# Performance work log

Measured on AMD Instinct MI355X. Metric: run time of the kernel, lower is better.

Reference implementation:

```python
import jax, jax.numpy as jnp
import numpy as np

S = 4            # n_streams
SINK_ITERS = 20
EPS = 1e-8
LN_EPS = 1e-5


def sinkhorn_knopp(logits):
    # Project onto doubly stochastic manifold (fixed 20 iterations, tiny SxS matrix)
    P = jnp.exp(logits - jnp.max(logits))
    for _ in range(SINK_ITERS):
        P = P / (jnp.sum(P, axis=-1, keepdims=True) + EPS)
        P = P / (jnp.sum(P, axis=-2, keepdims=True) + EPS)
    return P


def layer_norm(x, gamma, beta):
    mu = jnp.mean(x, axis=-1, keepdims=True)
    var = jnp.mean(jnp.square(x - mu), axis=-1, keepdims=True)
    return (x - mu) * jax.lax.rsqrt(var + LN_EPS) * gamma + beta


def mhc_residual(x_s, layer_s, H_res_logits, H_post_logits, scales):
    # x_{l+1} streams = H_res @ x + H_post.T @ layer_output (per-stream mixing)
    H_res = sinkhorn_knopp(H_res_logits)
    H_post = jax.nn.softmax(H_post_logits, axis=-1)
    residual = jnp.einsum('bnsd,st->bntd', x_s, H_res)
    mixed = jnp.einsum('bnsd,ts->bntd', layer_s, H_post)
    return residual + scales[None, None, :, None] * mixed


def setup_inputs() -> dict:
    key = jax.random.key(0)
    ks = jax.random.split(key, 10)
    B, N, D = 4, 4096, 2048
    scale_w = 1.0 / np.sqrt(D)
    return {
        'x': jax.random.normal(ks[0], (B, N, D), jnp.float32),
        'ln_gamma': jnp.ones((D,), jnp.float32),
        'ln_beta': jnp.zeros((D,), jnp.float32),
        'W_attn': jax.random.normal(ks[1], (D, D), jnp.float32) * scale_w,
        'b_attn': jnp.zeros((D,), jnp.float32),
        'W_hyb': jax.random.normal(ks[2], (D, D), jnp.float32) * scale_w,
        'b_hyb': jnp.zeros((D,), jnp.float32),
        'H_pre_attn_logits': 0.02 * jax.random.normal(ks[3], (S, S), jnp.float32),
        'H_pre_hyb_logits': 0.02 * jax.random.normal(ks[4], (S, S), jnp.float32),
        'H_res_attn_logits': jnp.eye(S, dtype=jnp.float32) + 0.1 * jax.random.normal(ks[5], (S, S), jnp.float32),
        'H_post_attn_logits': 0.02 * jax.random.normal(ks[6], (S, S), jnp.float32),
        'scales_attn': jnp.ones((S,), jnp.float32),
        'H_res_hyb_logits': jnp.eye(S, dtype=jnp.float32) + 0.1 * jax.random.normal(ks[7], (S, S), jnp.float32),
        'H_post_hyb_logits': 0.02 * jax.random.normal(ks[8], (S, S), jnp.float32),
        'scales_hyb': jnp.ones((S,), jnp.float32),
        'cross_mix': jnp.float32(0.5),
    }


def reference(x, ln_gamma, ln_beta, W_attn, b_attn, W_hyb, b_hyb,
              H_pre_attn_logits, H_pre_hyb_logits,
              H_res_attn_logits, H_post_attn_logits, scales_attn,
              H_res_hyb_logits, H_post_hyb_logits, scales_hyb, cross_mix):
    B, N, D = x.shape
    sd = D // S
    x_s = x.reshape(B, N, S, sd)

    # --- attention path: H_pre on LayerNorm-ed input ---
    normed_s = layer_norm(x, ln_gamma, ln_beta).reshape(B, N, S, sd)
    H_pre_attn = jax.nn.softmax(H_pre_attn_logits, axis=-1)
    attn_in = jnp.einsum('bnsd,st->bntd', normed_s, H_pre_attn).reshape(B, N, D)
    attn_out = attn_in @ W_attn + b_attn                  # attn_module stand-in
    x_attn = mhc_residual(x_s, attn_out.reshape(B, N, S, sd),
                          H_res_attn_logits, H_post_attn_logits, scales_attn)

    # --- hybrid path: H_pre on raw x ---
    H_pre_hyb = jax.nn.softmax(H_pre_hyb_logits, axis=-1)
    hyb_in = jnp.einsum('bnsd,st->bntd', x_s, H_pre_hyb).reshape(B, N, D)
    ssm_out = hyb_in @ W_hyb + b_hyb                      # hybrid_module stand-in
    x_hyb = mhc_residual(x_s, ssm_out.reshape(B, N, S, sd),
                         H_res_hyb_logits, H_post_hyb_logits, scales_hyb)

    alpha = jax.nn.sigmoid(cross_mix)
    out = alpha * x_attn + (1.0 - alpha) * x_hyb
    return out.reshape(B, N, D)
```

## Files before the change

kernel.cpp:

```cpp
#include <hip/hip_runtime.h>
#include <stdint.h>

typedef float  f32x4  __attribute__((ext_vector_type(4)));
typedef short  bf16x8 __attribute__((ext_vector_type(8)));
typedef unsigned short u16;
typedef unsigned short u16x8 __attribute__((ext_vector_type(8)));

#define GLD16(gsrc, ldst) \
  __builtin_amdgcn_global_load_lds((const __attribute__((address_space(1))) uint32_t*)(gsrc), \
                                   (__attribute__((address_space(3))) uint32_t*)(ldst), 16, 0, 0)

static __device__ __forceinline__ u16 f2bf(float f) {
  union { float f; uint32_t u; } v; v.f = f;
  uint32_t r = (v.u + 0x7FFFu + ((v.u >> 16) & 1u)) >> 16;
  return (u16)r;
}

__global__ void k_prep(const float* __restrict__ HpreA_l, const float* __restrict__ HpreH_l,
                       const float* __restrict__ HresA_l, const float* __restrict__ HpostA_l,
                       const float* __restrict__ scalesA,
                       const float* __restrict__ HresH_l, const float* __restrict__ HpostH_l,
                       const float* __restrict__ scalesH,
                       const float* __restrict__ crossmix, float* __restrict__ consts) {
  if (threadIdx.x != 0) return;
  float alpha = 1.0f / (1.0f + expf(-crossmix[0]));
  float Pa[16], Ph[16], SA[16], SH[16], QA[16], QH[16];
  const float* Ls[4] = {HpreA_l, HpreH_l, HpostA_l, HpostH_l};
  float* Os[4] = {Pa, Ph, QA, QH};
  for (int m = 0; m < 4; ++m) {
    for (int r = 0; r < 4; ++r) {
      float mx = Ls[m][r*4+0];
      for (int c = 1; c < 4; ++c) mx = fmaxf(mx, Ls[m][r*4+c]);
      float s = 0.f;
      for (int c = 0; c < 4; ++c) { float e = expf(Ls[m][r*4+c] - mx); Os[m][r*4+c] = e; s += e; }
      for (int c = 0; c < 4; ++c) Os[m][r*4+c] /= s;
    }
  }
  const float* Lr[2] = {HresA_l, HresH_l};
  float* Or[2] = {SA, SH};
  for (int m = 0; m < 2; ++m) {
    float mx = Lr[m][0];
    for (int i = 1; i < 16; ++i) mx = fmaxf(mx, Lr[m][i]);
    for (int i = 0; i < 16; ++i) Or[m][i] = expf(Lr[m][i] - mx);
    for (int it = 0; it < 20; ++it) {
      for (int r = 0; r < 4; ++r) {
        float s = 1e-8f;
        for (int c = 0; c < 4; ++c) s += Or[m][r*4+c];
        for (int c = 0; c < 4; ++c) Or[m][r*4+c] /= s;
      }
      for (int c = 0; c < 4; ++c) {
        float s = 1e-8f;
        for (int r = 0; r < 4; ++r) s += Or[m][r*4+c];
        for (int r = 0; r < 4; ++r) Or[m][r*4+c] /= s;
      }
    }
  }
  for (int i = 0; i < 16; ++i) consts[i]      = Pa[i];
  for (int i = 0; i < 16; ++i) consts[16 + i] = Ph[i];
  for (int i = 0; i < 16; ++i) consts[32 + i] = alpha * SA[i] + (1.0f - alpha) * SH[i];
  for (int t = 0; t < 4; ++t)
    for (int s = 0; s < 4; ++s) {
      consts[48 + t*4 + s] = alpha * scalesA[t] * QA[t*4 + s];
      consts[64 + t*4 + s] = (1.0f - alpha) * scalesH[t] * QH[t*4 + s];
    }
}

__global__ void k_bias(const float* __restrict__ bA, const float* __restrict__ bH,
                       const float* __restrict__ consts, float* __restrict__ bias) {
  int j = blockIdx.x * 256 + threadIdx.x;
  int t = j >> 9, d = j & 511;
  float acc = 0.f;
  for (int s = 0; s < 4; ++s)
    acc += consts[48 + t*4 + s] * bA[s*512 + d] + consts[64 + t*4 + s] * bH[s*512 + d];
  bias[j] = acc;
}

__global__ __launch_bounds__(256) void k_fold(const float* __restrict__ Wa,
                                              const float* __restrict__ Wh,
                                              const float* __restrict__ consts,
                                              float* __restrict__ temp) {
  int bid  = blockIdx.x;
  int da   = bid >> 2;
  int half = (bid >> 1) & 1;
  int j4   = (bid & 1) * 256 + threadIdx.x;
  int t    = j4 >> 7;
  int dcol = (j4 & 127) * 4;
  const float* W  = half ? Wh : Wa;
  const float* Hp = consts + (half ? 16 : 0);
  const float* C  = consts + (half ? 64 : 48);
  float c_t[4];
  for (int s = 0; s < 4; ++s) c_t[s] = C[t*4 + s];
  f32x4 acc[4];
  for (int p = 0; p < 4; ++p) for (int e = 0; e < 4; ++e) acc[p][e] = 0.f;
  #pragma unroll
  for (int u = 0; u < 4; ++u) {
    float hp[4];
    for (int p = 0; p < 4; ++p) hp[p] = Hp[p*4 + u];
    #pragma unroll
    for (int s = 0; s < 4; ++s) {
      f32x4 wv = *(const f32x4*)&W[(size_t)(u*512 + da) * 2048 + s*512 + dcol];
      float cs = c_t[s];
      for (int p = 0; p < 4; ++p) acc[p] += (hp[p] * cs) * wv;
    }
  }
  if (half) {
    int e = da - dcol;
    if (e >= 0 && e < 4)
      for (int p = 0; p < 4; ++p) acc[p][e] += consts[32 + p*4 + t];
  }
  for (int p = 0; p < 4; ++p)
    *(f32x4*)&temp[(size_t)(half*2048 + p*512 + da) * 2048 + j4*4] = acc[p];
}

__global__ __launch_bounds__(256) void k_transpose(const float* __restrict__ temp,
                                                   u16* __restrict__ Bt) {
  __shared__ float tile[64][65];
  int r0 = blockIdx.x * 64;
  int c0 = blockIdx.y * 64;
  int tid = threadIdx.x;
  int lr = tid >> 4;
  int lc = (tid & 15) * 4;
  #pragma unroll
  for (int i = 0; i < 4; ++i) {
    int row = lr + i * 16;
    f32x4 v = *(const f32x4*)&temp[(size_t)(r0 + row) * 2048 + c0 + lc];
    tile[row][lc+0] = v[0]; tile[row][lc+1] = v[1];
    tile[row][lc+2] = v[2]; tile[row][lc+3] = v[3];
  }
  __syncthreads();
  #pragma unroll
  for (int k = 0; k < 4; ++k) {
    int jj = lr + k * 16;
    ushort4 o;
    o.x = f2bf(tile[lc+0][jj]); o.y = f2bf(tile[lc+1][jj]);
    o.z = f2bf(tile[lc+2][jj]); o.w = f2bf(tile[lc+3][jj]);
    *(ushort4*)&Bt[(size_t)(c0 + jj) * 4096 + r0 + lc] = o;
  }
}

__global__ __launch_bounds__(256) void k_rowprep(const float* __restrict__ x,
                                                 const float* __restrict__ gamma,
                                                 const float* __restrict__ beta,
                                                 u16* __restrict__ A) {
  int m = blockIdx.x;
  int tid = threadIdx.x;
  const float* row = x + (size_t)m * 2048;
  f32x4 v0 = *(const f32x4*)&row[tid*8];
  f32x4 v1 = *(const f32x4*)&row[tid*8 + 4];
  float s1 = v0[0]+v0[1]+v0[2]+v0[3] + v1[0]+v1[1]+v1[2]+v1[3];
  float s2 = v0[0]*v0[0]+v0[1]*v0[1]+v0[2]*v0[2]+v0[3]*v0[3]
           + v1[0]*v1[0]+v1[1]*v1[1]+v1[2]*v1[2]+v1[3]*v1[3];
  for (int off = 32; off > 0; off >>= 1) {
    s1 += __shfl_down(s1, off);
    s2 += __shfl_down(s2, off);
  }
  __shared__ float red[8];
  int w = tid >> 6, l = tid & 63;
  if (l == 0) { red[w] = s1; red[4 + w] = s2; }
  __syncthreads();
  float t1 = red[0]+red[1]+red[2]+red[3];
  float t2 = red[4]+red[5]+red[6]+red[7];
  float mu = t1 * (1.0f/2048.0f);
  float var = t2 * (1.0f/2048.0f) - mu*mu;
  float rstd = rsqrtf(var + 1e-5f);
  f32x4 g0 = *(const f32x4*)&gamma[tid*8];
  f32x4 g1 = *(const f32x4*)&gamma[tid*8 + 4];
  f32x4 b0 = *(const f32x4*)&beta[tid*8];
  f32x4 b1 = *(const f32x4*)&beta[tid*8 + 4];
  u16x8 pn, pr;
  #pragma unroll
  for (int e = 0; e < 4; ++e) {
    pr[e]   = f2bf(v0[e]);
    pr[4+e] = f2bf(v1[e]);
    pn[e]   = f2bf((v0[e] - mu) * rstd * g0[e] + b0[e]);
    pn[4+e] = f2bf((v1[e] - mu) * rstd * g1[e] + b1[e]);
  }
  *(u16x8*)&A[(size_t)m * 4096 + tid*8]        = pn;
  *(u16x8*)&A[(size_t)m * 4096 + 2048 + tid*8] = pr;
}

__global__ __launch_bounds__(256) void k_gemm(const u16* __restrict__ A,
                                              const u16* __restrict__ B,
                                              const float* __restrict__ bias,
                                              float* __restrict__ out) {
  __shared__ __align__(16) u16 ldsA[128 * 32];
  __shared__ __align__(16) u16 ldsB[128 * 32];
  int bid = blockIdx.x;
  int mt = bid >> 4, nt = bid & 15;
  int m0 = mt * 128, n0 = nt * 128;
  int tid = threadIdx.x;
  int l = tid & 63, w = tid >> 6;
  int lr = l & 15, lk = l >> 4;
  int wm = (w >> 1) * 64, wn = (w & 1) * 64;
  const char* gA = (const char*)A + (size_t)m0 * 8192;
  const char* gB = (const char*)B + (size_t)n0 * 8192;
  char* lA = (char*)ldsA;
  char* lB = (char*)ldsB;

  f32x4 acc[4][4];
  for (int mi = 0; mi < 4; ++mi)
    for (int ni = 0; ni < 4; ++ni)
      for (int r = 0; r < 4; ++r) acc[mi][ni][r] = 0.f;

  for (int kt = 0; kt < 128; ++kt) {
    #pragma unroll
    for (int c = 0; c < 2; ++c) {
      int ob = (w * 2 + c) * 1024;
      int o  = ob + l * 16;
      int rw = o >> 6;
      int kb = o & 63;
      GLD16(gA + (size_t)rw * 8192 + kt * 64 + kb, lA + ob);
      GLD16(gB + (size_t)rw * 8192 + kt * 64 + kb, lB + ob);
    }
    __syncthreads();
    bf16x8 af[4], bfr[4];
    #pragma unroll
    for (int mi = 0; mi < 4; ++mi)
      af[mi] = *(const bf16x8*)(lA + (wm + mi*16 + lr) * 64 + lk * 16);
    #pragma unroll
    for (int ni = 0; ni < 4; ++ni)
      bfr[ni] = *(const bf16x8*)(lB + (wn + ni*16 + lr) * 64 + lk * 16);
    #pragma unroll
    for (int mi = 0; mi < 4; ++mi)
      #pragma unroll
      for (int ni = 0; ni < 4; ++ni)
        acc[mi][ni] = __builtin_amdgcn_mfma_f32_16x16x32_bf16(af[mi], bfr[ni], acc[mi][ni], 0, 0, 0);
    __syncthreads();
  }

  #pragma unroll
  for (int ni = 0; ni < 4; ++ni) {
    int col = n0 + wn + ni*16 + lr;
    float bc = bias[col];
    #pragma unroll
    for (int mi = 0; mi < 4; ++mi)
      #pragma unroll
      for (int r = 0; r < 4; ++r) {
        int row = m0 + wm + mi*16 + lk*4 + r;
        out[(size_t)row * 2048 + col] = acc[mi][ni][r] + bc;
      }
  }
}

__global__ void k_report(float* out, float v) {
  out[blockIdx.x * 256 + threadIdx.x] = v;
}

extern "C" void kernel_launch(void* const* d_in, const int* in_sizes, int n_in,
                              void* d_out, int out_size, void* d_ws, size_t ws_size,
                              hipStream_t stream) {
  (void)in_sizes; (void)n_in; (void)out_size;
  const float* x       = (const float*)d_in[0];
  const float* gamma   = (const float*)d_in[1];
  const float* beta    = (const float*)d_in[2];
  const float* Wa      = (const float*)d_in[3];
  const float* ba      = (const float*)d_in[4];
  const float* Wh      = (const float*)d_in[5];
  const float* bh      = (const float*)d_in[6];
  const float* HpreA   = (const float*)d_in[7];
  const float* HpreH   = (const float*)d_in[8];
  const float* HresA   = (const float*)d_in[9];
  const float* HpostA  = (const float*)d_in[10];
  const float* scalesA = (const float*)d_in[11];
  const float* HresH   = (const float*)d_in[12];
  const float* HpostH  = (const float*)d_in[13];
  const float* scalesH = (const float*)d_in[14];
  const float* cm      = (const float*)d_in[15];
  float* out = (float*)d_out;

  const size_t OFF_CONST = 0;
  const size_t OFF_BIAS  = 4096;
  const size_t OFF_B     = (size_t)1 << 20;
  const size_t OFF_A     = (size_t)17 << 20;
  const size_t NEED      = OFF_A + ((size_t)128 << 20);

  if (ws_size < NEED) {
    k_report<<<4, 256, 0, stream>>>(out, (float)(ws_size >> 20));
    return;
  }

  float* consts = (float*)((char*)d_ws + OFF_CONST);
  float* bias   = (float*)((char*)d_ws + OFF_BIAS);
  u16*   Bt     = (u16*)((char*)d_ws + OFF_B);
  u16*   Am     = (u16*)((char*)d_ws + OFF_A);
  float* temp   = (float*)((char*)d_ws + OFF_A);

  k_prep<<<1, 64, 0, stream>>>(HpreA, HpreH, HresA, HpostA, scalesA,
                               HresH, HpostH, scalesH, cm, consts);
  k_bias<<<8, 256, 0, stream>>>(ba, bh, consts, bias);
  k_fold<<<2048, 256, 0, stream>>>(Wa, Wh, consts, temp);
  k_transpose<<<dim3(64, 32), 256, 0, stream>>>(temp, Bt);
  k_rowprep<<<16384, 256, 0, stream>>>(x, gamma, beta, Am);
  k_gemm<<<2048, 256, 0, stream>>>(Am, Bt, bias, out);
}
```

Measured before the change: 666.8 us.

## Replace GEMM with 256x256 pipelined 8-wave kernel and merge prep kernels

Replaces the 128x128 single-buffered GEMM with a 256x256-tile, 512-thread kernel. It double-buffers LDS via async global-to-LDS loads, XOR-swizzles LDS rows to avoid bank conflicts, raises MFMA priority with setprio, and swizzles block order for L2 reuse. It also fuses the constant-prep and bias kernels into one launch and rewrites row prep so each wave handles one row without block-level reduction. The intent is higher MFMA utilisation through more data reuse and overlap of loads with compute, at the cost of more registers and barriers, with occupancy limited to 2 blocks per CU.

```diff
diff --git a/kernel.cpp b/kernel.cpp
--- a/kernel.cpp
+++ b/kernel.cpp
@@ -16,63 +16,68 @@
   return (u16)r;
 }
 
-__global__ void k_prep(const float* __restrict__ HpreA_l, const float* __restrict__ HpreH_l,
-                       const float* __restrict__ HresA_l, const float* __restrict__ HpostA_l,
-                       const float* __restrict__ scalesA,
-                       const float* __restrict__ HresH_l, const float* __restrict__ HpostH_l,
-                       const float* __restrict__ scalesH,
-                       const float* __restrict__ crossmix, float* __restrict__ consts) {
-  if (threadIdx.x != 0) return;
-  float alpha = 1.0f / (1.0f + expf(-crossmix[0]));
-  float Pa[16], Ph[16], SA[16], SH[16], QA[16], QH[16];
-  const float* Ls[4] = {HpreA_l, HpreH_l, HpostA_l, HpostH_l};
-  float* Os[4] = {Pa, Ph, QA, QH};
-  for (int m = 0; m < 4; ++m) {
-    for (int r = 0; r < 4; ++r) {
-      float mx = Ls[m][r*4+0];
-      for (int c = 1; c < 4; ++c) mx = fmaxf(mx, Ls[m][r*4+c]);
-      float s = 0.f;
-      for (int c = 0; c < 4; ++c) { float e = expf(Ls[m][r*4+c] - mx); Os[m][r*4+c] = e; s += e; }
-      for (int c = 0; c < 4; ++c) Os[m][r*4+c] /= s;
-    }
-  }
-  const float* Lr[2] = {HresA_l, HresH_l};
-  float* Or[2] = {SA, SH};
-  for (int m = 0; m < 2; ++m) {
-    float mx = Lr[m][0];
-    for (int i = 1; i < 16; ++i) mx = fmaxf(mx, Lr[m][i]);
-    for (int i = 0; i < 16; ++i) Or[m][i] = expf(Lr[m][i] - mx);
-    for (int it = 0; it < 20; ++it) {
+__global__ void k_prepbias(const float* __restrict__ HpreA_l, const float* __restrict__ HpreH_l,
+                           const float* __restrict__ HresA_l, const float* __restrict__ HpostA_l,
+                           const float* __restrict__ scalesA,
+                           const float* __restrict__ HresH_l, const float* __restrict__ HpostH_l,
+                           const float* __restrict__ scalesH,
+                           const float* __restrict__ crossmix, float* __restrict__ consts,
+                           const float* __restrict__ bA, const float* __restrict__ bH,
+                           float* __restrict__ bias) {
+  __shared__ float sc[80];
+  if (threadIdx.x == 0) {
+    float alpha = 1.0f / (1.0f + expf(-crossmix[0]));
+    float Pa[16], Ph[16], SA[16], SH[16], QA[16], QH[16];
+    const float* Ls[4] = {HpreA_l, HpreH_l, HpostA_l, HpostH_l};
+    float* Os[4] = {Pa, Ph, QA, QH};
+    for (int m = 0; m < 4; ++m) {
       for (int r = 0; r < 4; ++r) {
-        float s = 1e-8f;
-        for (int c = 0; c < 4; ++c) s += Or[m][r*4+c];
-        for (int c = 0; c < 4; ++c) Or[m][r*4+c] /= s;
-      }
-      for (int c = 0; c < 4; ++c) {
-        float s = 1e-8f;
-        for (int r = 0; r < 4; ++r) s += Or[m][r*4+c];
-        for (int r = 0; r < 4; ++r) Or[m][r*4+c] /= s;
+        float mx = Ls[m][r*4+0];
+        for (int c = 1; c < 4; ++c) mx = fmaxf(mx, Ls[m][r*4+c]);
+        float s = 0.f;
+        for (int c = 0; c < 4; ++c) { float e = expf(Ls[m][r*4+c] - mx); Os[m][r*4+c] = e; s += e; }
+        for (int c = 0; c < 4; ++c) Os[m][r*4+c] /= s;
       }
     }
-  }
-  for (int i = 0; i < 16; ++i) consts[i]      = Pa[i];
-  for (int i = 0; i < 16; ++i) consts[16 + i] = Ph[i];
-  for (int i = 0; i < 16; ++i) consts[32 + i] = alpha * SA[i] + (1.0f - alpha) * SH[i];
-  for (int t = 0; t < 4; ++t)
-    for (int s = 0; s < 4; ++s) {
-      consts[48 + t*4 + s] = alpha * scalesA[t] * QA[t*4 + s];
-      consts[64 + t*4 + s] = (1.0f - alpha) * scalesH[t] * QH[t*4 + s];
+    const float* Lr[2] = {HresA_l, HresH_l};
+    float* Or[2] = {SA, SH};
+    for (int m = 0; m < 2; ++m) {
+      float mx = Lr[m][0];
+      for (int i = 1; i < 16; ++i) mx = fmaxf(mx, Lr[m][i]);
+      for (int i = 0; i < 16; ++i) Or[m][i] = expf(Lr[m][i] - mx);
+      for (int it = 0; it < 20; ++it) {
+        for (int r = 0; r < 4; ++r) {
+          float s = 1e-8f;
+          for (int c = 0; c < 4; ++c) s += Or[m][r*4+c];
+          for (int c = 0; c < 4; ++c) Or[m][r*4+c] /= s;
+        }
+        for (int c = 0; c < 4; ++c) {
+          float s = 1e-8f;
+          for (int r = 0; r < 4; ++r) s += Or[m][r*4+c];
+          for (int r = 0; r < 4; ++r) Or[m][r*4+c] /= s;
+        }
+      }
     }
-}
-
-__global__ void k_bias(const float* __restrict__ bA, const float* __restrict__ bH,
-                       const float* __restrict__ consts, float* __restrict__ bias) {
-  int j = blockIdx.x * 256 + threadIdx.x;
-  int t = j >> 9, d = j & 511;
-  float acc = 0.f;
-  for (int s = 0; s < 4; ++s)
-    acc += consts[48 + t*4 + s] * bA[s*512 + d] + consts[64 + t*4 + s] * bH[s*512 + d];
-  bias[j] = acc;
+    for (int i = 0; i < 16; ++i) sc[i]      = Pa[i];
+    for (int i = 0; i < 16; ++i) sc[16 + i] = Ph[i];
+    for (int i = 0; i < 16; ++i) sc[32 + i] = alpha * SA[i] + (1.0f - alpha) * SH[i];
+    for (int t = 0; t < 4; ++t)
+      for (int s = 0; s < 4; ++s) {
+        sc[48 + t*4 + s] = alpha * scalesA[t] * QA[t*4 + s];
+        sc[64 + t*4 + s] = (1.0f - alpha) * scalesH[t] * QH[t*4 + s];
+      }
+    for (int i = 0; i < 80; ++i) consts[i] = sc[i];
+  }
+  __syncthreads();
+  #pragma unroll
+  for (int k = 0; k < 8; ++k) {
+    int j = k*256 + threadIdx.x;
+    int t = j >> 9, d = j & 511;
+    float acc = 0.f;
+    for (int s = 0; s < 4; ++s)
+      acc += sc[48 + t*4 + s] * bA[s*512 + d] + sc[64 + t*4 + s] * bH[s*512 + d];
+    bias[j] = acc;
+  }
 }
 
 __global__ __launch_bounds__(256) void k_fold(const float* __restrict__ Wa,
@@ -142,103 +147,202 @@
                                                  const float* __restrict__ gamma,
                                                  const float* __restrict__ beta,
                                                  u16* __restrict__ A) {
-  int m = blockIdx.x;
+  int wid = (blockIdx.x * 256 + threadIdx.x) >> 6;
+  int l = threadIdx.x & 63;
+  const float* row = x + (size_t)wid * 2048;
+  f32x4 v[8];
+  float s1 = 0.f, s2 = 0.f;
+  #pragma unroll
+  for (int j = 0; j < 8; ++j) {
+    v[j] = *(const f32x4*)&row[j*256 + l*4];
+    #pragma unroll
+    for (int e = 0; e < 4; ++e) { s1 += v[j][e]; s2 += v[j][e]*v[j][e]; }
+  }
+  #pragma unroll
+  for (int off = 32; off; off >>= 1) {
+    s1 += __shfl_down(s1, off, 64);
+    s2 += __shfl_down(s2, off, 64);
+  }
+  s1 = __shfl(s1, 0, 64);
+  s2 = __shfl(s2, 0, 64);
+  float mu   = s1 * (1.0f/2048.0f);
+  float var  = s2 * (1.0f/2048.0f) - mu*mu;
+  float rstd = rsqrtf(var + 1e-5f);
+  u16* An = A + (size_t)wid * 4096;
+  #pragma unroll
+  for (int j = 0; j < 8; ++j) {
+    f32x4 g = *(const f32x4*)&gamma[j*256 + l*4];
+    f32x4 b = *(const f32x4*)&beta[j*256 + l*4];
+    ushort4 pn, pr;
+    pn.x = f2bf((v[j][0]-mu)*rstd*g[0] + b[0]);
+    pn.y = f2bf((v[j][1]-mu)*rstd*g[1] + b[1]);
+    pn.z = f2bf((v[j][2]-mu)*rstd*g[2] + b[2]);
+    pn.w = f2bf((v[j][3]-mu)*rstd*g[3] + b[3]);
+    pr.x = f2bf(v[j][0]); pr.y = f2bf(v[j][1]);
+    pr.z = f2bf(v[j][2]); pr.w = f2bf(v[j][3]);
+    *(ushort4*)&An[j*256 + l*4]        = pn;
+    *(ushort4*)&An[2048 + j*256 + l*4] = pr;
+  }
+}
+
+
+static __device__ __forceinline__ void read4(bf16x8* F, const char* base) {
+  #pragma unroll
+  for (int i = 0; i < 4; ++i) F[i] = *(const bf16x8*)(base + i*1024);
+}
+static __device__ __forceinline__ void mfma16(f32x4 (*accq)[4], const bf16x8* Af, const bf16x8* Bf) {
+  __builtin_amdgcn_s_setprio(1);
+  #pragma unroll
+  for (int j = 0; j < 4; ++j)
+    #pragma unroll
+    for (int ni = 0; ni < 4; ++ni)
+      accq[j][ni] = __builtin_amdgcn_mfma_f32_16x16x32_bf16(Af[j], Bf[ni], accq[j][ni], 0, 0, 0);
+  __builtin_amdgcn_s_setprio(0);
+}
+
+#define STAGE_A(ktt, h, dt) { const char* g_ = gA + (ktt)*128 + (h)*64; \
+  char* s_ = lA + ((dt)*2 + (h))*16384; GLD16(g_ + go0, s_ + lo0); GLD16(g_ + go1, s_ + lo1); }
+#define STAGE_B(ktt, h, dt) { const char* g_ = gB + (ktt)*128 + (h)*64; \
+  char* s_ = lB + ((dt)*2 + (h))*16384; GLD16(g_ + go0, s_ + lo0); GLD16(g_ + go1, s_ + lo1); }
+#define VM(n) { asm volatile("s_waitcnt vmcnt(" #n ")" ::: "memory"); __builtin_amdgcn_sched_barrier(0); }
+#define BAR() __builtin_amdgcn_s_barrier()
+
+__global__ __launch_bounds__(512, 2) void k_gemm8(const u16* __restrict__ A,
+                                                  const u16* __restrict__ B,
+                                                  const float* __restrict__ bias,
+                                                  float* __restrict__ out) {
+  __shared__ __align__(16) u16 ldsA[2*2*256*32];
+  __shared__ __align__(16) u16 ldsB[2*2*256*32];
+  int bid = blockIdx.x;
+  int swz = (bid & 7) * 64 + (bid >> 3);
+  int mt = swz >> 3, nt = swz & 7;
+  int m0 = mt * 256, n0 = nt * 256;
   int tid = threadIdx.x;
-  const float* row = x + (size_t)m * 2048;
-  f32x4 v0 = *(const f32x4*)&row[tid*8];
-  f32x4 v1 = *(const f32x4*)&row[tid*8 + 4];
-  float s1 = v0[0]+v0[1]+v0[2]+v0[3] + v1[0]+v1[1]+v1[2]+v1[3];
-  float s2 = v0[0]*v0[0]+v0[1]*v0[1]+v0[2]*v0[2]+v0[3]*v0[3]
-           + v1[0]*v1[0]+v1[1]*v1[1]+v1[2]*v1[2]+v1[3]*v1[3];
-  for (int off = 32; off > 0; off >>= 1) {
-    s1 += __shfl_down(s1, off);
-    s2 += __shfl_down(s2, off);
-  }
-  __shared__ float red[8];
   int w = tid >> 6, l = tid & 63;
-  if (l == 0) { red[w] = s1; red[4 + w] = s2; }
-  __syncthreads();
-  float t1 = red[0]+red[1]+red[2]+red[3];
-  float t2 = red[4]+red[5]+red[6]+red[7];
-  float mu = t1 * (1.0f/2048.0f);
-  float var = t2 * (1.0f/2048.0f) - mu*mu;
-  float rstd = rsqrtf(var + 1e-5f);
-  f32x4 g0 = *(const f32x4*)&gamma[tid*8];
-  f32x4 g1 = *(const f32x4*)&gamma[tid*8 + 4];
-  f32x4 b0 = *(const f32x4*)&beta[tid*8];
-  f32x4 b1 = *(const f32x4*)&beta[tid*8 + 4];
-  u16x8 pn, pr;
-  #pragma unroll
-  for (int e = 0; e < 4; ++e) {
-    pr[e]   = f2bf(v0[e]);
-    pr[4+e] = f2bf(v1[e]);
-    pn[e]   = f2bf((v0[e] - mu) * rstd * g0[e] + b0[e]);
-    pn[4+e] = f2bf((v1[e] - mu) * rstd * g1[e] + b1[e]);
-  }
-  *(u16x8*)&A[(size_t)m * 4096 + tid*8]        = pn;
-  *(u16x8*)&A[(size_t)m * 4096 + 2048 + tid*8] = pr;
-}
-
-__global__ __launch_bounds__(256) void k_gemm(const u16* __restrict__ A,
-                                              const u16* __restrict__ B,
-                                              const float* __restrict__ bias,
-                                              float* __restrict__ out) {
-  __shared__ __align__(16) u16 ldsA[128 * 32];
-  __shared__ __align__(16) u16 ldsB[128 * 32];
-  int bid = blockIdx.x;
-  int mt = bid >> 4, nt = bid & 15;
-  int m0 = mt * 128, n0 = nt * 128;
-  int tid = threadIdx.x;
-  int l = tid & 63, w = tid >> 6;
+  int wr = w >> 2, wc = w & 3;
   int lr = l & 15, lk = l >> 4;
-  int wm = (w >> 1) * 64, wn = (w & 1) * 64;
   const char* gA = (const char*)A + (size_t)m0 * 8192;
   const char* gB = (const char*)B + (size_t)n0 * 8192;
   char* lA = (char*)ldsA;
   char* lB = (char*)ldsB;
 
-  f32x4 acc[4][4];
-  for (int mi = 0; mi < 4; ++mi)
+  int ch0 = w*64 + l, ch1 = 512 + w*64 + l;
+  size_t go0 = (size_t)(ch0 >> 2) * 8192 + (size_t)((((ch0 & 3) ^ ((ch0 >> 4) & 3))) << 4);
+  size_t go1 = (size_t)(ch1 >> 2) * 8192 + (size_t)((((ch1 & 3) ^ ((ch1 >> 4) & 3))) << 4);
+  int lo0 = w * 1024, lo1 = 8192 + w * 1024;
+
+  int rsw = (lr >> 2) & 3;
+  int aoff = (wr*128 + lr) * 64 + ((lk ^ rsw) << 4);
+  int boff = (wc*64  + lr) * 64 + ((lk ^ rsw) << 4);
+
+  f32x4 acc[8][4];
+  #pragma unroll
+  for (int mi = 0; mi < 8; ++mi)
+    #pragma unroll
     for (int ni = 0; ni < 4; ++ni)
-      for (int r = 0; r < 4; ++r) acc[mi][ni][r] = 0.f;
-
-  for (int kt = 0; kt < 128; ++kt) {
-    #pragma unroll
-    for (int c = 0; c < 2; ++c) {
-      int ob = (w * 2 + c) * 1024;
-      int o  = ob + l * 16;
-      int rw = o >> 6;
-      int kb = o & 63;
-      GLD16(gA + (size_t)rw * 8192 + kt * 64 + kb, lA + ob);
-      GLD16(gB + (size_t)rw * 8192 + kt * 64 + kb, lB + ob);
+      #pragma unroll
+      for (int e = 0; e < 4; ++e) acc[mi][ni][e] = 0.f;
+
+  STAGE_A(0, 0, 0); STAGE_B(0, 0, 0);
+  STAGE_A(0, 1, 0); STAGE_B(0, 1, 0);
+  STAGE_A(1, 0, 1); STAGE_B(1, 0, 1);
+  VM(8);
+  BAR();
+
+  const int NT = 64;
+  for (int kt = 0; kt < NT-2; ++kt) {
+    int d = kt & 1, dn = d ^ 1;
+    int h0 = (d*2 + 0) * 16384, h1 = (d*2 + 1) * 16384;
+    bf16x8 Af[4], Bf[4];
+    read4(Bf, lB + h0 + boff);
+    read4(Af, lA + h0 + aoff);
+    STAGE_A(kt+1, 1, dn);
+    BAR();
+    mfma16(&acc[0], Af, Bf);
+    BAR();
+    read4(Af, lA + h0 + aoff + 4096);
+    STAGE_B(kt+1, 1, dn);
+    BAR();
+    mfma16(&acc[4], Af, Bf);
+    VM(8);
+    BAR();
+    read4(Bf, lB + h1 + boff);
+    read4(Af, lA + h1 + aoff);
+    STAGE_A(kt+2, 0, d);
+    BAR();
+    mfma16(&acc[0], Af, Bf);
+    BAR();
+    read4(Af, lA + h1 + aoff + 4096);
+    STAGE_B(kt+2, 0, d);
+    BAR();
+    mfma16(&acc[4], Af, Bf);
+    VM(8);
+    BAR();
+  }
+  {
+    const int kt = NT-2;
+    int d = kt & 1, dn = d ^ 1;
+    int h0 = (d*2 + 0) * 16384, h1 = (d*2 + 1) * 16384;
+    bf16x8 Af[4], Bf[4];
+    read4(Bf, lB + h0 + boff);
+    read4(Af, lA + h0 + aoff);
+    STAGE_A(kt+1, 1, dn);
+    BAR();
+    mfma16(&acc[0], Af, Bf);
+    BAR();
+    read4(Af, lA + h0 + aoff + 4096);
+    STAGE_B(kt+1, 1, dn);
+    BAR();
+    mfma16(&acc[4], Af, Bf);
+    VM(8);
+    BAR();
+    read4(Bf, lB + h1 + boff);
+    read4(Af, lA + h1 + aoff);
+    BAR();
+    mfma16(&acc[0], Af, Bf);
+    BAR();
+    read4(Af, lA + h1 + aoff + 4096);
+    BAR();
+    mfma16(&acc[4], Af, Bf);
+    VM(4);
+    BAR();
+  }
+  {
+    const int kt = NT-1;
+    int d = kt & 1;
+    int h0 = (d*2 + 0) * 16384, h1 = (d*2 + 1) * 16384;
+    bf16x8 Af[4], Bf[4];
+    read4(Bf, lB + h0 + boff);
+    read4(Af, lA + h0 + aoff);
+    BAR();
+    mfma16(&acc[0], Af, Bf);
+    BAR();
+    read4(Af, lA + h0 + aoff + 4096);
+    BAR();
+    mfma16(&acc[4], Af, Bf);
+    VM(0);
+    BAR();
+    read4(Bf, lB + h1 + boff);
+    read4(Af, lA + h1 + aoff);
+    BAR();
+    mfma16(&acc[0], Af, Bf);
+    BAR();
+    read4(Af, lA + h1 + aoff + 4096);
+    BAR();
+    mfma16(&acc[4], Af, Bf);
+  }
+
+  #pragma unroll
+  for (int ni = 0; ni < 4; ++ni) {
+    int col = n0 + wc*64 + ni*16 + lr;
+    float bc = bias[col];
+    #pragma unroll
+    for (int mi = 0; mi < 8; ++mi) {
+      int row = m0 + wr*128 + mi*16 + lk*4;
+      #pragma unroll
+      for (int e = 0; e < 4; ++e)
+        out[(size_t)(row + e) * 2048 + col] = acc[mi][ni][e] + bc;
     }
-    __syncthreads();
-    bf16x8 af[4], bfr[4];
-    #pragma unroll
-    for (int mi = 0; mi < 4; ++mi)
-      af[mi] = *(const bf16x8*)(lA + (wm + mi*16 + lr) * 64 + lk * 16);
-    #pragma unroll
-    for (int ni = 0; ni < 4; ++ni)
-      bfr[ni] = *(const bf16x8*)(lB + (wn + ni*16 + lr) * 64 + lk * 16);
-    #pragma unroll
-    for (int mi = 0; mi < 4; ++mi)
-      #pragma unroll
-      for (int ni = 0; ni < 4; ++ni)
-        acc[mi][ni] = __builtin_amdgcn_mfma_f32_16x16x32_bf16(af[mi], bfr[ni], acc[mi][ni], 0, 0, 0);
-    __syncthreads();
-  }
-
-  #pragma unroll
-  for (int ni = 0; ni < 4; ++ni) {
-    int col = n0 + wn + ni*16 + lr;
-    float bc = bias[col];
-    #pragma unroll
-    for (int mi = 0; mi < 4; ++mi)
-      #pragma unroll
-      for (int r = 0; r < 4; ++r) {
-        int row = m0 + wm + mi*16 + lk*4 + r;
-        out[(size_t)row * 2048 + col] = acc[mi][ni][r] + bc;
-      }
   }
 }
 
@@ -285,11 +389,10 @@
   u16*   Am     = (u16*)((char*)d_ws + OFF_A);
   float* temp   = (float*)((char*)d_ws + OFF_A);
 
-  k_prep<<<1, 64, 0, stream>>>(HpreA, HpreH, HresA, HpostA, scalesA,
-                               HresH, HpostH, scalesH, cm, consts);
-  k_bias<<<8, 256, 0, stream>>>(ba, bh, consts, bias);
+  k_prepbias<<<1, 256, 0, stream>>>(HpreA, HpreH, HresA, HpostA, scalesA,
+                                    HresH, HpostH, scalesH, cm, consts, ba, bh, bias);
   k_fold<<<2048, 256, 0, stream>>>(Wa, Wh, consts, temp);
   k_transpose<<<dim3(64, 32), 256, 0, stream>>>(temp, Bt);
-  k_rowprep<<<16384, 256, 0, stream>>>(x, gamma, beta, Am);
-  k_gemm<<<2048, 256, 0, stream>>>(Am, Bt, bias, out);
-}
+  k_rowprep<<<4096, 256, 0, stream>>>(x, gamma, beta, Am);
+  k_gemm8<<<512, 512, 0, stream>>>(Am, Bt, bias, out);
+}
```

After: 642.5 us. -3.6%, faster.
